# Kernel tuning notes

Measured on AMD Instinct MI355X. Metric: run time of the kernel, lower is better.

## Reference

```python
import jax, jax.numpy as jnp
import numpy as np


def setup_inputs() -> dict:
    key = jax.random.key(0)
    ks = jax.random.split(key, 6)
    B, H, W, C = 4, 56, 56, 256
    NH, K = 8, 7
    return {
        "x": jax.random.normal(ks[0], (B, H, W, C), dtype=jnp.float32),
        "w_qkv": jax.random.normal(ks[1], (C, 3 * C), dtype=jnp.float32) * 0.02,
        "b_qkv": jax.random.normal(ks[2], (3 * C,), dtype=jnp.float32) * 0.02,
        "rpb": jax.random.normal(ks[3], (NH, K * K), dtype=jnp.float32) * 0.02,
        "w_proj": jax.random.normal(ks[4], (C, C), dtype=jnp.float32) * 0.02,
        "b_proj": jax.random.normal(ks[5], (C,), dtype=jnp.float32) * 0.02,
    }


def _window_stack(xp, H, W, ks):
    # xp: (B, H+2p, W+2p, nh, hd) zero-padded map.
    # Returns (B, H, W, nh, ks*ks, hd): each pixel's ks x ks neighborhood,
    # row-major (h offset outer, w offset inner) to match torch unfold order.
    return jnp.stack(
        [xp[:, i:i + H, j:j + W] for i in range(ks) for j in range(ks)],
        axis=-2,
    )


def reference(x, w_qkv, b_qkv, rpb, w_proj, b_proj):
    B, H, W, C = x.shape
    nh, ks2 = rpb.shape
    ks = int(np.sqrt(ks2) + 0.5)  # 7
    hd = C // nh
    scale = hd ** -0.5
    pad = ks // 2  # dilation == 1

    qkv = (x @ w_qkv + b_qkv).reshape(B, H, W, 3, nh, hd)
    q = qkv[..., 0, :, :] * scale        # (B,H,W,nh,hd)
    k = qkv[..., 1, :, :]
    v = qkv[..., 2, :, :]

    pads = ((0, 0), (pad, pad), (pad, pad), (0, 0), (0, 0))
    kw = _window_stack(jnp.pad(k, pads), H, W, ks)  # (B,H,W,nh,ks2,hd)
    vw = _window_stack(jnp.pad(v, pads), H, W, ks)

    # scores over each pixel's ks*ks neighbors (zero-padded borders kept,
    # matching the torch reference), plus relative position bias.
    attn = jnp.einsum("bhwnd,bhwnkd->bhwnk", q, kw) + rpb[None, None, None]
    attn = jax.nn.softmax(attn, axis=-1)
    out = jnp.einsum("bhwnk,bhwnkd->bhwnd", attn, vw).reshape(B, H, W, C)
    return out @ w_proj + b_proj
```

## Files before the change

### kernel.cpp

```cpp
#include <hip/hip_runtime.h>
#include <hip/hip_bf16.h>


using frag_ab = __attribute__((ext_vector_type(8))) short;
using f32x4   = __attribute__((ext_vector_type(4))) float;
using f32x2   = __attribute__((ext_vector_type(2))) float;

typedef const __attribute__((address_space(1))) unsigned int* gas_u32;
typedef __attribute__((address_space(3))) unsigned int*       las_u32;

__device__ __forceinline__ void gl_lds16(const void* g, void* l) {
    __builtin_amdgcn_global_load_lds((gas_u32)g, (las_u32)l, 16, 0, 0);
}

__device__ __forceinline__ float bflo(unsigned int u) { return __uint_as_float(u << 16); }
__device__ __forceinline__ float bfhi(unsigned int u) { return __uint_as_float(u & 0xffff0000u); }

__device__ __forceinline__ f32x2 unpk2(unsigned int u) {
    f32x2 r; r.x = bflo(u); r.y = bfhi(u); return r;
}

#if defined(__has_builtin)
#if __has_builtin(__builtin_amdgcn_fdot2_f32_bf16)
#define HAVE_FDOT2_BF16 1
#endif
#endif

#ifdef HAVE_FDOT2_BF16
typedef __bf16 bf16x2 __attribute__((ext_vector_type(2)));
__device__ __forceinline__ float dot2bf(unsigned int a, unsigned int b, float c) {
    union { unsigned int u; bf16x2 h; } ua, ub;
    ua.u = a; ub.u = b;
    return __builtin_amdgcn_fdot2_f32_bf16(ua.h, ub.h, c, false);
}
#endif

__global__ __launch_bounds__(256) void prep_k(
    const float* __restrict__ x,      __hip_bfloat16* __restrict__ xb,
    const float* __restrict__ w_qkv,  __hip_bfloat16* __restrict__ wqkvT,
    const float* __restrict__ w_proj, __hip_bfloat16* __restrict__ wprojT,
    __hip_bfloat16* __restrict__ kp,  __hip_bfloat16* __restrict__ vp)
{
    const int bid = blockIdx.x;
    const int tid = threadIdx.x;
    if (bid < 3136) {
        const int i = bid * 256 + tid;
        const float4 v = ((const float4*)x)[i];
        union { ushort4 u; __hip_bfloat16 h[4]; } o;
        o.h[0] = __float2bfloat16(v.x); o.h[1] = __float2bfloat16(v.y);
        o.h[2] = __float2bfloat16(v.z); o.h[3] = __float2bfloat16(v.w);
        ((ushort4*)xb)[i] = o.u;
    } else if (bid < 3904) {
        const int idx = (bid - 3136) * 256 + tid;
        const int k = idx & 255, n = idx >> 8;
        wqkvT[idx] = __float2bfloat16(w_qkv[k * 768 + n]);
    } else if (bid < 4160) {
        const int idx = (bid - 3904) * 256 + tid;
        const int k = idx & 255, n = idx >> 8;
        wprojT[idx] = __float2bfloat16(w_proj[k * 256 + n]);
    } else {
        const int u    = (bid - 4160) * 256 + tid;
        const int ip   = u / 30720;
        const int rem  = u - ip * 30720;
        const int cloc = rem >> 5;
        const int q16  = rem & 31;
        const int img  = ip >> 1;
        __hip_bfloat16* base = (ip & 1) ? vp : kp;
        int prow, pcol;
        if (cloc < 512) {
            const int r8 = cloc >> 6;
            prow = (r8 < 3) ? r8 : r8 + 56;
            pcol = cloc & 63;
        } else {
            const int c2 = cloc - 512;
            prow = 3 + (c2 >> 3);
            const int cc = c2 & 7;
            pcol = (cc < 3) ? cc : cc + 56;
        }
        *(uint4*)(base + (((size_t)(img * 64 + prow)) * 64 + pcol) * 256 + q16 * 8) =
            make_uint4(0u, 0u, 0u, 0u);
    }
}

__global__ __launch_bounds__(256) void gemm_qkv_k(
    const __hip_bfloat16* __restrict__ A,
    const __hip_bfloat16* __restrict__ BT,
    const float* __restrict__ bias,
    __hip_bfloat16* __restrict__ qf,
    __hip_bfloat16* __restrict__ kp,
    __hip_bfloat16* __restrict__ vp,
    float qscale)
{
    constexpr int K = 256;
    __shared__ frag_ab As[4][64];
    __shared__ frag_ab Bs[8][64];

    const int tid  = threadIdx.x;
    const int lane = tid & 63;
    const int w    = tid >> 6;
    const int wm   = w >> 1, wn = w & 1;
    const int m0 = blockIdx.y * 64;
    const int n0 = blockIdx.x * 128;

    const int lrow = lane & 15;
    const int lk   = (lane >> 4) * 8;
    const __hip_bfloat16* gA  = A  + (size_t)(m0 + w * 16 + lrow) * K + lk;
    const __hip_bfloat16* gB0 = BT + (size_t)(n0 + (2*w+0)*16 + lrow) * K + lk;
    const __hip_bfloat16* gB1 = BT + (size_t)(n0 + (2*w+1)*16 + lrow) * K + lk;

    f32x4 acc[2][4] = {};

    for (int k0 = 0; k0 < K; k0 += 32) {
        gl_lds16(gA  + k0, &As[w][0]);
        gl_lds16(gB0 + k0, &Bs[2*w+0][0]);
        gl_lds16(gB1 + k0, &Bs[2*w+1][0]);
        __syncthreads();
        frag_ab af[2], bf[4];
        #pragma unroll
        for (int i = 0; i < 2; ++i) af[i] = As[2*wm + i][lane];
        #pragma unroll
        for (int j = 0; j < 4; ++j) bf[j] = Bs[wn*4 + j][lane];
        #pragma unroll
        for (int i = 0; i < 2; ++i)
            #pragma unroll
            for (int j = 0; j < 4; ++j)
                acc[i][j] = __builtin_amdgcn_mfma_f32_16x16x32_bf16(af[i], bf[j], acc[i][j], 0, 0, 0);
        __syncthreads();
    }

    const int sel  = n0 >> 8;
    const int rbase = (lane >> 4) * 4;
    const int cbase = lane & 15;
    __hip_bfloat16* dstp = (sel == 1) ? kp : vp;

    #pragma unroll
    for (int fi = 0; fi < 2; ++fi) {
        #pragma unroll
        for (int r = 0; r < 4; ++r) {
            const int mm = m0 + wm * 32 + fi * 16 + rbase + r;
            size_t rowbase;
            if (sel == 0) {
                rowbase = (size_t)mm * 256;
            } else {
                const int bb = mm / 3136;
                const int r2 = mm % 3136;
                const int yy = r2 / 56;
                const int xx = r2 % 56;
                rowbase = (((size_t)(bb * 64 + yy + 3)) * 64 + (xx + 3)) * 256;
            }
            #pragma unroll
            for (int fj = 0; fj < 4; ++fj) {
                const int cn = n0 + wn * 64 + fj * 16 + cbase;
                const float val = acc[fi][fj][r] + bias[cn];
                if (sel == 0) {
                    qf[rowbase + cn] = __float2bfloat16(val * qscale);
                } else {
                    dstp[rowbase + (cn & 255)] = __float2bfloat16(val);
                }
            }
        }
    }
}

__global__ __launch_bounds__(256) void gemm_proj_k(
    const __hip_bfloat16* __restrict__ A,
    const __hip_bfloat16* __restrict__ BT,
    const float* __restrict__ bias,
    float* __restrict__ C)
{
    constexpr int K = 256;
    __shared__ frag_ab As[4][64];
    __shared__ frag_ab Bs[4][64];

    const int tid  = threadIdx.x;
    const int lane = tid & 63;
    const int w    = tid >> 6;
    const int wm   = w >> 1, wn = w & 1;
    const int m0 = blockIdx.y * 64;
    const int n0 = blockIdx.x * 64;

    const int lrow = lane & 15;
    const int lk   = (lane >> 4) * 8;
    const __hip_bfloat16* gA = A  + (size_t)(m0 + w * 16 + lrow) * K + lk;
    const __hip_bfloat16* gB = BT + (size_t)(n0 + w * 16 + lrow) * K + lk;

    f32x4 acc[2][2] = {};

    for (int k0 = 0; k0 < K; k0 += 32) {
        gl_lds16(gA + k0, &As[w][0]);
        gl_lds16(gB + k0, &Bs[w][0]);
        __syncthreads();
        const frag_ab a0 = As[2 * wm + 0][lane];
        const frag_ab a1 = As[2 * wm + 1][lane];
        const frag_ab b0 = Bs[2 * wn + 0][lane];
        const frag_ab b1 = Bs[2 * wn + 1][lane];
        acc[0][0] = __builtin_amdgcn_mfma_f32_16x16x32_bf16(a0, b0, acc[0][0], 0, 0, 0);
        acc[0][1] = __builtin_amdgcn_mfma_f32_16x16x32_bf16(a0, b1, acc[0][1], 0, 0, 0);
        acc[1][0] = __builtin_amdgcn_mfma_f32_16x16x32_bf16(a1, b0, acc[1][0], 0, 0, 0);
        acc[1][1] = __builtin_amdgcn_mfma_f32_16x16x32_bf16(a1, b1, acc[1][1], 0, 0, 0);
        __syncthreads();
    }

    const int rbase = (lane >> 4) * 4;
    const int cbase = lane & 15;
    #pragma unroll
    for (int fi = 0; fi < 2; ++fi) {
        const int rm = m0 + wm * 32 + fi * 16 + rbase;
        #pragma unroll
        for (int fj = 0; fj < 2; ++fj) {
            const int cn = n0 + wn * 32 + fj * 16 + cbase;
            const float bv = bias[cn];
            #pragma unroll
            for (int r = 0; r < 4; ++r)
                C[(size_t)(rm + r) * 256 + cn] = acc[fi][fj][r] + bv;
        }
    }
}

__global__ __launch_bounds__(256) void na2d_attn_k(
    const __hip_bfloat16* __restrict__ qf,
    const __hip_bfloat16* __restrict__ kp,
    const __hip_bfloat16* __restrict__ vp,
    const float* __restrict__ rpb,
    __hip_bfloat16* __restrict__ out)
{
    const int tid  = threadIdx.x;
    const int lane = tid & 63;
    const int wv   = tid >> 6;
    const int q8   = lane & 3;
    const int h    = (lane >> 2) & 7;
    const int tl   = (lane >> 5) & 1;

    const int bid = blockIdx.x;
    const int seg = (bid & 7) * 784 + (bid >> 3) * 4 + wv;
    const int row = seg / 28;
    const int x0  = (seg % 28) * 2;
    const int b   = row / 56;
    const int y   = row % 56;
    const int t   = row * 56 + x0 + tl;
    const int prow0 = b * 64 + y;

    __shared__ __hip_bfloat16 kbuf4[4][8 * 256];
    __shared__ float srpb[8 * 49];
    __hip_bfloat16* kbuf = kbuf4[wv];

    for (int i = tid; i < 8 * 49; i += 256) srpb[i] = rpb[i];
    __syncthreads();

    unsigned int qpk[4];
    {
        const uint4 qa = *(const uint4*)(qf + (size_t)t * 256 + h * 32 + q8 * 8);
        qpk[0] = qa.x; qpk[1] = qa.y; qpk[2] = qa.z; qpk[3] = qa.w;
    }
#ifndef HAVE_FDOT2_BF16
    f32x2 q2[4];
    #pragma unroll
    for (int i = 0; i < 4; ++i) q2[i] = unpk2(qpk[i]);
#endif

    const int wroff = lane * 16;
    const int rdoff = tl * 512 + h * 64 + q8 * 16;

#define GLOAD4(plane, ky, d0, d1, d2, d3)                                       \
    do {                                                                        \
        const char* rb_ = (const char*)((plane) +                               \
            ((size_t)(prow0 + (ky)) * 64 + x0) * 256 + lane * 8);               \
        d0 = *(const uint4*)(rb_);                                              \
        d1 = *(const uint4*)(rb_ + 1024);                                       \
        d2 = *(const uint4*)(rb_ + 2048);                                       \
        d3 = *(const uint4*)(rb_ + 3072);                                       \
    } while (0)

#define LWRITE4(buf, s0, s1, s2, s3)                                            \
    do {                                                                        \
        char* wb_ = (char*)(buf) + wroff;                                       \
        *(uint4*)(wb_)        = s0;                                             \
        *(uint4*)(wb_ + 1024) = s1;                                             \
        *(uint4*)(wb_ + 2048) = s2;                                             \
        *(uint4*)(wb_ + 3072) = s3;                                             \
    } while (0)

    const float* rp = &srpb[h * 49];
    float m = -1e30f, l = 0.f;
    f32x2 o2[4] = {};

    uint4 k0, k1, k2, k3;
    GLOAD4(kp, 0, k0, k1, k2, k3);

    #pragma unroll 1
    for (int ky = 0; ky < 7; ++ky) {
        LWRITE4(kbuf, k0, k1, k2, k3);
        const __hip_bfloat16* vrow = vp +
            ((size_t)(prow0 + ky) * 64 + x0 + tl) * 256 + h * 32 + q8 * 8;
        uint4 va[7];
        #pragma unroll
        for (int kx = 0; kx < 7; ++kx)
            va[kx] = *(const uint4*)(vrow + kx * 256);
        if (ky < 6) GLOAD4(kp, ky + 1, k0, k1, k2, k3);
        float lg[7];
        #pragma unroll
        for (int kx = 0; kx < 7; ++kx) {
            const uint4 w0 = *(const uint4*)((const char*)kbuf + rdoff + kx * 512);
#ifdef HAVE_FDOT2_BF16
            float s = 0.f;
            s = dot2bf(qpk[0], w0.x, s);
            s = dot2bf(qpk[1], w0.y, s);
            s = dot2bf(qpk[2], w0.z, s);
            s = dot2bf(qpk[3], w0.w, s);
#else
            f32x2 s2 = {0.f, 0.f};
            s2 += q2[0] * unpk2(w0.x);
            s2 += q2[1] * unpk2(w0.y);
            s2 += q2[2] * unpk2(w0.z);
            s2 += q2[3] * unpk2(w0.w);
            const float s = s2.x + s2.y;
#endif
            lg[kx] = s;
        }
        #pragma unroll
        for (int kx = 0; kx < 7; ++kx) {
            lg[kx] += __shfl_xor(lg[kx], 1, 64);
            lg[kx] += __shfl_xor(lg[kx], 2, 64);
            lg[kx] += rp[ky * 7 + kx];
        }
        float rmax = lg[0];
        #pragma unroll
        for (int kx = 1; kx < 7; ++kx) rmax = fmaxf(rmax, lg[kx]);
        const float mnew  = fmaxf(m, rmax);
        const float alpha = __expf(m - mnew);
        m = mnew;
        l *= alpha;
        const f32x2 alpha2 = {alpha, alpha};
        #pragma unroll
        for (int i = 0; i < 4; ++i) o2[i] *= alpha2;
        #pragma unroll
        for (int kx = 0; kx < 7; ++kx) {
            const float pr = __expf(lg[kx] - mnew);
            l += pr;
            const f32x2 pr2 = {pr, pr};
            const uint4 w0 = va[kx];
            o2[0] += pr2 * unpk2(w0.x);
            o2[1] += pr2 * unpk2(w0.y);
            o2[2] += pr2 * unpk2(w0.z);
            o2[3] += pr2 * unpk2(w0.w);
        }
    }
#undef GLOAD4
#undef LWRITE4

    const float inv = 1.f / l;
    union { uint4 u; __hip_bfloat16 hh[8]; } ob;
    #pragma unroll
    for (int i = 0; i < 4; ++i) {
        ob.hh[2 * i + 0] = __float2bfloat16(o2[i].x * inv);
        ob.hh[2 * i + 1] = __float2bfloat16(o2[i].y * inv);
    }
    *(uint4*)(out + (size_t)t * 256 + h * 32 + q8 * 8) = ob.u;
}

extern "C" void kernel_launch(void* const* d_in, const int* in_sizes, int n_in,
                              void* d_out, int out_size, void* d_ws, size_t ws_size,
                              hipStream_t stream)
{
    const float* x      = (const float*)d_in[0];
    const float* w_qkv  = (const float*)d_in[1];
    const float* b_qkv  = (const float*)d_in[2];
    const float* rpb    = (const float*)d_in[3];
    const float* w_proj = (const float*)d_in[4];
    const float* b_proj = (const float*)d_in[5];
    float* out = (float*)d_out;

    const int M = 12544;

    char* wsp = (char*)d_ws;
    __hip_bfloat16* qf    = (__hip_bfloat16*)wsp; wsp += (size_t)M * 256 * 2;
    __hip_bfloat16* kp    = (__hip_bfloat16*)wsp; wsp += (size_t)4 * 64 * 64 * 256 * 2;
    __hip_bfloat16* vp    = (__hip_bfloat16*)wsp; wsp += (size_t)4 * 64 * 64 * 256 * 2;
    __hip_bfloat16* xb    = (__hip_bfloat16*)wsp; wsp += (size_t)M * 256 * 2;
    __hip_bfloat16* attnb = (__hip_bfloat16*)wsp; wsp += (size_t)M * 256 * 2;
    __hip_bfloat16* wqkvT = (__hip_bfloat16*)wsp; wsp += (size_t)768 * 256 * 2;
    __hip_bfloat16* wprojT= (__hip_bfloat16*)wsp; wsp += (size_t)256 * 256 * 2;

    const float scale = 0.17677669529663689f;

    prep_k<<<5120, 256, 0, stream>>>(x, xb, w_qkv, wqkvT, w_proj, wprojT, kp, vp);

    gemm_qkv_k<<<dim3(6, 196), 256, 0, stream>>>(xb, wqkvT, b_qkv, qf, kp, vp, scale);

    na2d_attn_k<<<1568, 256, 0, stream>>>(qf, kp, vp, rpb, attnb);

    gemm_proj_k<<<dim3(4, 196), 256, 0, stream>>>(attnb, wprojT, b_proj, out);
}
```

Measured before the change: 131.6 us.

## Fuse output projection GEMM into neighborhood attention kernel epilogue

Drops the separate projection GEMM kernel and the bf16 attention-output buffer. Each attention block stages its 8 output rows in LDS, padded to a 16-row MFMA tile with zeros. Each wave then computes 64 output columns with MFMA, reading wprojT straight from global memory. This saves a kernel launch and a round trip of the intermediate through memory. The cost is that half of each MFMA tile is padding, and every block re-reads the full projection weight (128 KB) from L2.

```diff
diff --git a/kernel.cpp b/kernel.cpp
--- a/kernel.cpp
+++ b/kernel.cpp
@@ -162,67 +162,14 @@
     }
 }
 
-__global__ __launch_bounds__(256) void gemm_proj_k(
-    const __hip_bfloat16* __restrict__ A,
-    const __hip_bfloat16* __restrict__ BT,
-    const float* __restrict__ bias,
-    float* __restrict__ C)
-{
-    constexpr int K = 256;
-    __shared__ frag_ab As[4][64];
-    __shared__ frag_ab Bs[4][64];
-
-    const int tid  = threadIdx.x;
-    const int lane = tid & 63;
-    const int w    = tid >> 6;
-    const int wm   = w >> 1, wn = w & 1;
-    const int m0 = blockIdx.y * 64;
-    const int n0 = blockIdx.x * 64;
-
-    const int lrow = lane & 15;
-    const int lk   = (lane >> 4) * 8;
-    const __hip_bfloat16* gA = A  + (size_t)(m0 + w * 16 + lrow) * K + lk;
-    const __hip_bfloat16* gB = BT + (size_t)(n0 + w * 16 + lrow) * K + lk;
-
-    f32x4 acc[2][2] = {};
-
-    for (int k0 = 0; k0 < K; k0 += 32) {
-        gl_lds16(gA + k0, &As[w][0]);
-        gl_lds16(gB + k0, &Bs[w][0]);
-        __syncthreads();
-        const frag_ab a0 = As[2 * wm + 0][lane];
-        const frag_ab a1 = As[2 * wm + 1][lane];
-        const frag_ab b0 = Bs[2 * wn + 0][lane];
-        const frag_ab b1 = Bs[2 * wn + 1][lane];
-        acc[0][0] = __builtin_amdgcn_mfma_f32_16x16x32_bf16(a0, b0, acc[0][0], 0, 0, 0);
-        acc[0][1] = __builtin_amdgcn_mfma_f32_16x16x32_bf16(a0, b1, acc[0][1], 0, 0, 0);
-        acc[1][0] = __builtin_amdgcn_mfma_f32_16x16x32_bf16(a1, b0, acc[1][0], 0, 0, 0);
-        acc[1][1] = __builtin_amdgcn_mfma_f32_16x16x32_bf16(a1, b1, acc[1][1], 0, 0, 0);
-        __syncthreads();
-    }
-
-    const int rbase = (lane >> 4) * 4;
-    const int cbase = lane & 15;
-    #pragma unroll
-    for (int fi = 0; fi < 2; ++fi) {
-        const int rm = m0 + wm * 32 + fi * 16 + rbase;
-        #pragma unroll
-        for (int fj = 0; fj < 2; ++fj) {
-            const int cn = n0 + wn * 32 + fj * 16 + cbase;
-            const float bv = bias[cn];
-            #pragma unroll
-            for (int r = 0; r < 4; ++r)
-                C[(size_t)(rm + r) * 256 + cn] = acc[fi][fj][r] + bv;
-        }
-    }
-}
-
-__global__ __launch_bounds__(256) void na2d_attn_k(
+__global__ __launch_bounds__(256) void na2d_attn_proj_k(
     const __hip_bfloat16* __restrict__ qf,
     const __hip_bfloat16* __restrict__ kp,
     const __hip_bfloat16* __restrict__ vp,
     const float* __restrict__ rpb,
-    __hip_bfloat16* __restrict__ out)
+    const __hip_bfloat16* __restrict__ wprojT,
+    const float* __restrict__ b_proj,
+    float* __restrict__ out)
 {
     const int tid  = threadIdx.x;
     const int lane = tid & 63;
@@ -232,7 +179,8 @@
     const int tl   = (lane >> 5) & 1;
 
     const int bid = blockIdx.x;
-    const int seg = (bid & 7) * 784 + (bid >> 3) * 4 + wv;
+    const int segBase = (bid & 7) * 784 + (bid >> 3) * 4;
+    const int seg = segBase + wv;
     const int row = seg / 28;
     const int x0  = (seg % 28) * 2;
     const int b   = row / 56;
@@ -242,9 +190,12 @@
 
     __shared__ __hip_bfloat16 kbuf4[4][8 * 256];
     __shared__ float srpb[8 * 49];
+    __shared__ __align__(16) char abuf[16 * 528];
     __hip_bfloat16* kbuf = kbuf4[wv];
 
     for (int i = tid; i < 8 * 49; i += 256) srpb[i] = rpb[i];
+    for (int u = tid; u < 264; u += 256)
+        *(uint4*)(abuf + 4224 + u * 16) = make_uint4(0u, 0u, 0u, 0u);
     __syncthreads();
 
     unsigned int qpk[4];
@@ -348,14 +299,52 @@
 #undef GLOAD4
 #undef LWRITE4
 
-    const float inv = 1.f / l;
-    union { uint4 u; __hip_bfloat16 hh[8]; } ob;
-    #pragma unroll
-    for (int i = 0; i < 4; ++i) {
-        ob.hh[2 * i + 0] = __float2bfloat16(o2[i].x * inv);
-        ob.hh[2 * i + 1] = __float2bfloat16(o2[i].y * inv);
-    }
-    *(uint4*)(out + (size_t)t * 256 + h * 32 + q8 * 8) = ob.u;
+    {
+        const float inv = 1.f / l;
+        union { uint4 u; __hip_bfloat16 hh[8]; } ob;
+        #pragma unroll
+        for (int i = 0; i < 4; ++i) {
+            ob.hh[2 * i + 0] = __float2bfloat16(o2[i].x * inv);
+            ob.hh[2 * i + 1] = __float2bfloat16(o2[i].y * inv);
+        }
+        *(uint4*)(abuf + (wv * 2 + tl) * 528 + h * 64 + q8 * 16) = ob.u;
+    }
+    __syncthreads();
+
+    {
+        const int lrow = lane & 15;
+        const int lk   = (lane >> 4) * 8;
+        f32x4 pacc[4] = {};
+        const __hip_bfloat16* gBp = wprojT + (size_t)(wv * 64 + lrow) * 256 + lk;
+
+        #pragma unroll 2
+        for (int c = 0; c < 8; ++c) {
+            const frag_ab a = *(const frag_ab*)(abuf + lrow * 528 + c * 64 + lk * 2);
+            #pragma unroll
+            for (int j = 0; j < 4; ++j) {
+                const frag_ab bfr = *(const frag_ab*)(gBp + (size_t)j * 16 * 256 + c * 32);
+                pacc[j] = __builtin_amdgcn_mfma_f32_16x16x32_bf16(a, bfr, pacc[j], 0, 0, 0);
+            }
+        }
+
+        const int rbase = (lane >> 4) * 4;
+        const int cb    = lane & 15;
+        if (rbase < 8) {
+            float bv[4];
+            #pragma unroll
+            for (int j = 0; j < 4; ++j) bv[j] = b_proj[wv * 64 + j * 16 + cb];
+            #pragma unroll
+            for (int r = 0; r < 4; ++r) {
+                const int r8 = rbase + r;
+                const int sg = segBase + (r8 >> 1);
+                const int tt = (sg / 28) * 56 + (sg % 28) * 2 + (r8 & 1);
+                float* orow = out + (size_t)tt * 256 + wv * 64 + cb;
+                #pragma unroll
+                for (int j = 0; j < 4; ++j)
+                    orow[j * 16] = pacc[j][r] + bv[j];
+            }
+        }
+    }
 }
 
 extern "C" void kernel_launch(void* const* d_in, const int* in_sizes, int n_in,
@@ -377,7 +366,6 @@
     __hip_bfloat16* kp    = (__hip_bfloat16*)wsp; wsp += (size_t)4 * 64 * 64 * 256 * 2;
     __hip_bfloat16* vp    = (__hip_bfloat16*)wsp; wsp += (size_t)4 * 64 * 64 * 256 * 2;
     __hip_bfloat16* xb    = (__hip_bfloat16*)wsp; wsp += (size_t)M * 256 * 2;
-    __hip_bfloat16* attnb = (__hip_bfloat16*)wsp; wsp += (size_t)M * 256 * 2;
     __hip_bfloat16* wqkvT = (__hip_bfloat16*)wsp; wsp += (size_t)768 * 256 * 2;
     __hip_bfloat16* wprojT= (__hip_bfloat16*)wsp; wsp += (size_t)256 * 256 * 2;
 
@@ -387,7 +375,5 @@
 
     gemm_qkv_k<<<dim3(6, 196), 256, 0, stream>>>(xb, wqkvT, b_qkv, qf, kp, vp, scale);
 
-    na2d_attn_k<<<1568, 256, 0, stream>>>(qf, kp, vp, rpb, attnb);
-
-    gemm_proj_k<<<dim3(4, 196), 256, 0, stream>>>(attnb, wprojT, b_proj, out);
-}
+    na2d_attn_proj_k<<<1568, 256, 0, stream>>>(qf, kp, vp, rpb, wprojT, b_proj, out);
+}
```

After: 146.3 us. 11.2% more time.
